# Performance work log

Hardware: AMD Instinct MI355X
Metric: run time of the kernel (lower is better)

## Reference

```python
import jax, jax.numpy as jnp
import numpy as np

VOCAB, DM, H, DH, FF, NL = 50265, 768, 12, 64, 3072, 12
WIN = 256  # one-sided window (attention_window=512)
B, S = 1, 4096


def layer_norm(x, s, b, eps=1e-5):
    mu = x.mean(-1, keepdims=True)
    var = x.var(-1, keepdims=True)
    return (x - mu) * jax.lax.rsqrt(var + eps) * s + b


def sliding_attn(x, key_mask, wq, wk, wv, bq, bk, bv):
    Bb, Ss, _ = x.shape
    nb = Ss // WIN
    q = ((x @ wq + bq) / np.float32(np.sqrt(DH))).reshape(Bb, nb, WIN, H, DH)
    k = (x @ wk + bk).reshape(Bb, Ss, H, DH)
    v = (x @ wv + bv).reshape(Bb, Ss, H, DH)
    pad = [(0, 0), (WIN, WIN), (0, 0), (0, 0)]
    kp = jnp.pad(k, pad).reshape(Bb, nb + 2, WIN, H, DH)
    vp = jnp.pad(v, pad).reshape(Bb, nb + 2, WIN, H, DH)
    mp = jnp.pad(key_mask, [(0, 0), (WIN, WIN)]).reshape(Bb, nb + 2, WIN)
    kwin = jnp.concatenate([kp[:, i:i + nb] for i in range(3)], axis=2)  # [B,nb,3W,H,DH]
    vwin = jnp.concatenate([vp[:, i:i + nb] for i in range(3)], axis=2)
    mwin = jnp.concatenate([mp[:, i:i + nb] for i in range(3)], axis=2)  # [B,nb,3W]
    scores = jnp.einsum('bnqhd,bnkhd->bhnqk', q, kwin)  # [B,H,nb,W,3W]
    rel = jnp.arange(3 * WIN)[None, :] - jnp.arange(WIN)[:, None]
    band = (rel >= 0) & (rel <= 2 * WIN)
    valid = band[None, None, None] & (mwin > 0)[:, None, :, None, :]
    probs = jax.nn.softmax(jnp.where(valid, scores, -1e9), axis=-1)
    out = jnp.einsum('bhnqk,bnkhd->bnqhd', probs, vwin)
    return out.reshape(Bb, Ss, H * DH)


def encode(tokens, mask, word_emb, pos_emb, emb_ln_s, emb_ln_b, qkv_w, qkv_b,
           attn_out_w, attn_out_b, attn_ln_s, attn_ln_b,
           ffn_w1, ffn_b1, ffn_w2, ffn_b2, ffn_ln_s, ffn_ln_b):
    Ss = tokens.shape[1]
    x = word_emb[tokens] + pos_emb[2:2 + Ss][None]  # roberta-style position offset
    x = layer_norm(x, emb_ln_s, emb_ln_b)
    for l in range(NL):
        a = sliding_attn(x, mask, qkv_w[l, 0], qkv_w[l, 1], qkv_w[l, 2],
                         qkv_b[l, 0], qkv_b[l, 1], qkv_b[l, 2])
        x = layer_norm(x + a @ attn_out_w[l] + attn_out_b[l], attn_ln_s[l], attn_ln_b[l])
        h = jax.nn.gelu(x @ ffn_w1[l] + ffn_b1[l], approximate=False)
        x = layer_norm(x + h @ ffn_w2[l] + ffn_b2[l], ffn_ln_s[l], ffn_ln_b[l])
    return x


def setup_inputs() -> dict:
    key = jax.random.key(0)
    ks = iter(jax.random.split(key, 40))
    tokens = jax.random.randint(next(ks), (B, 1, S), 0, VOCAB)
    mask = jnp.ones((B, 1, S), dtype=jnp.int64 if False else jnp.int32)
    essay_tokens = jnp.concatenate([tokens, mask.astype(tokens.dtype)], axis=1)
    g = lambda shape: (jax.random.normal(next(ks), shape, jnp.float32) * 0.02)
    return {
        'essay_tokens': essay_tokens,
        'word_emb': g((VOCAB, DM)), 'pos_emb': g((4098, DM)),
        'emb_ln_s': jnp.ones((DM,)), 'emb_ln_b': jnp.zeros((DM,)),
        'qkv_w': g((NL, 3, DM, DM)), 'qkv_b': g((NL, 3, DM)),
        'attn_out_w': g((NL, DM, DM)), 'attn_out_b': g((NL, DM)),
        'attn_ln_s': jnp.ones((NL, DM)), 'attn_ln_b': jnp.zeros((NL, DM)),
        'ffn_w1': g((NL, DM, FF)), 'ffn_b1': g((NL, FF)),
        'ffn_w2': g((NL, FF, DM)), 'ffn_b2': g((NL, DM)),
        'ffn_ln_s': jnp.ones((NL, DM)), 'ffn_ln_b': jnp.zeros((NL, DM)),
        'cls_w1': g((DM, 512)), 'cls_b1': jnp.zeros((512,)),
        'cls_w2': g((512, 512)), 'cls_b2': jnp.zeros((512,)),
        'cls_w3': g((512, 512)), 'cls_b3': jnp.zeros((512,)),
        'cls_w4': g((512, 2)), 'cls_b4': jnp.zeros((2,)),
    }


def reference(essay_tokens, word_emb, pos_emb, emb_ln_s, emb_ln_b, qkv_w, qkv_b,
              attn_out_w, attn_out_b, attn_ln_s, attn_ln_b,
              ffn_w1, ffn_b1, ffn_w2, ffn_b2, ffn_ln_s, ffn_ln_b,
              cls_w1, cls_b1, cls_w2, cls_b2, cls_w3, cls_b3, cls_w4, cls_b4):
    tokens = essay_tokens[:, 0, :].astype(jnp.int32)
    mask = essay_tokens[:, 1, :].astype(jnp.int32)
    enc = encode(tokens, mask, word_emb, pos_emb, emb_ln_s, emb_ln_b, qkv_w, qkv_b,
                 attn_out_w, attn_out_b, attn_ln_s, attn_ln_b,
                 ffn_w1, ffn_b1, ffn_w2, ffn_b2, ffn_ln_s, ffn_ln_b)
    # torch.no_grad() on the transformer
    enc = jax.lax.stop_gradient(enc)
    h = enc @ cls_w1 + cls_b1
    h = h @ cls_w2 + cls_b2
    h = h @ cls_w3 + cls_b3
    logits = h @ cls_w4 + cls_b4  # [B,S,2]
    out = logits[..., 0]          # chunk(..., 2, dim=-1)[0] then flatten(1)
    return out.reshape(out.shape[0], -1)
```

## Files before the change

### kernel.cpp

```cpp
#include <hip/hip_runtime.h>
#include <cmath>

#define S_LEN 4096
#define DMODEL 768
#define NHEAD 12
#define DHEAD 64
#define FFDIM 3072
#define NLAYER 12
#define WINR 256

typedef float f32x4 __attribute__((ext_vector_type(4)));
typedef short s8v __attribute__((ext_vector_type(8)));
typedef __bf16 b8v __attribute__((ext_vector_type(8)));

__device__ __forceinline__ short f2b(float f) {
  unsigned u = __builtin_bit_cast(unsigned, f);
  unsigned r = (u + 0x7fffu + ((u >> 16) & 1u)) >> 16;
  return (short)r;
}
__device__ __forceinline__ float b2f(short s) {
  unsigned u = ((unsigned)(unsigned short)s) << 16;
  return __builtin_bit_cast(float, u);
}
__device__ __forceinline__ f32x4 mfma16(s8v a, s8v b, f32x4 c) {
  return __builtin_amdgcn_mfma_f32_16x16x32_bf16(
      __builtin_bit_cast(b8v, a), __builtin_bit_cast(b8v, b), c, 0, 0, 0);
}
__device__ __forceinline__ void gl_lds16(const short* g, short* l) {
  __builtin_amdgcn_global_load_lds(
      (const __attribute__((address_space(1))) unsigned int*)g,
      (__attribute__((address_space(3))) unsigned int*)l, 16, 0, 0);
}

#define QSCALE 0.18033688011112042f
#define THR2 11.5415603f

__device__ __forceinline__ void wtr_tile(const float* __restrict__ src,
                                         short* __restrict__ dst, int K, int N,
                                         int k0, int n0, int t,
                                         short (*tile)[65]) {
  {
    int kr = t >> 2, nc = (t & 3) * 16;
    const float* p = src + (long)(k0 + kr) * N + n0 + nc;
#pragma unroll
    for (int q = 0; q < 4; ++q) {
      float4 f = *(const float4*)(p + q * 4);
      tile[kr][nc + q * 4 + 0] = f2b(f.x);
      tile[kr][nc + q * 4 + 1] = f2b(f.y);
      tile[kr][nc + q * 4 + 2] = f2b(f.z);
      tile[kr][nc + q * 4 + 3] = f2b(f.w);
    }
  }
  __syncthreads();
  {
    int nr = t >> 2, cc = (t & 3) * 16;
    short* q = dst + (long)(n0 + nr) * K + k0 + cc;
    s8v v0, v1;
#pragma unroll
    for (int j = 0; j < 8; ++j) v0[j] = tile[cc + j][nr];
#pragma unroll
    for (int j = 0; j < 8; ++j) v1[j] = tile[cc + 8 + j][nr];
    *(s8v*)q = v0;
    *(s8v*)(q + 8) = v1;
  }
}

__global__ __launch_bounds__(256) void wtr_kernel(const float* __restrict__ src,
                                                  short* __restrict__ dst,
                                                  int K, int N) {
  __shared__ short tile[64][65];
  wtr_tile(src, dst, K, N, blockIdx.y * 64, blockIdx.x * 64, threadIdx.x, tile);
}

__global__ __launch_bounds__(256) void wtr_layer_kernel(
    const float* __restrict__ qkv, const float* __restrict__ ao,
    const float* __restrict__ w1, const float* __restrict__ w2,
    short* __restrict__ lwq, short* __restrict__ lwa, short* __restrict__ lw1,
    short* __restrict__ lw2) {
  __shared__ short tile[64][65];
  const long DD = (long)DMODEL * DMODEL;
  int id = blockIdx.x;
  const float* src;
  short* dst;
  int K, N, nT, kT;
  if (id < 432) {
    int m = id / 144, r = id % 144;
    src = qkv + m * DD; dst = lwq + m * DD;
    K = DMODEL; N = DMODEL; nT = r % 12; kT = r / 12;
  } else if (id < 576) {
    int r = id - 432;
    src = ao; dst = lwa;
    K = DMODEL; N = DMODEL; nT = r % 12; kT = r / 12;
  } else if (id < 1152) {
    int r = id - 576;
    src = w1; dst = lw1;
    K = DMODEL; N = FFDIM; nT = r % 48; kT = r / 48;
  } else {
    int r = id - 1152;
    src = w2; dst = lw2;
    K = FFDIM; N = DMODEL; nT = r % 12; kT = r / 12;
  }
  wtr_tile(src, dst, K, N, kT * 64, nT * 64, threadIdx.x, tile);
}

__global__ __launch_bounds__(256) void vtr_kernel(const short* __restrict__ Vb,
                                                  short* __restrict__ VTg) {
  __shared__ short tile[64][65];
  const int s0 = blockIdx.x * 64, h = blockIdx.y;
  const int t = threadIdx.x;
  {
    int sr = t >> 2, dc = (t & 3) * 16;
    const short* p = Vb + (long)(s0 + sr) * DMODEL + h * 64 + dc;
    s8v a0 = *(const s8v*)p;
    s8v a1 = *(const s8v*)(p + 8);
#pragma unroll
    for (int j = 0; j < 8; ++j) tile[sr][dc + j] = a0[j];
#pragma unroll
    for (int j = 0; j < 8; ++j) tile[sr][dc + 8 + j] = a1[j];
  }
  __syncthreads();
  {
    int dr = t >> 2, sc = (t & 3) * 16;
    short* q = VTg + (long)(h * 64 + dr) * S_LEN + s0 + sc;
    s8v v0, v1;
#pragma unroll
    for (int j = 0; j < 8; ++j) v0[j] = tile[sc + j][dr];
#pragma unroll
    for (int j = 0; j < 8; ++j) v1[j] = tile[sc + 8 + j][dr];
    *(s8v*)q = v0;
    *(s8v*)(q + 8) = v1;
  }
}

template <int EPI, int OUT>
__global__ __launch_bounds__(256, 4) void bgemm_kernel(
    const short* __restrict__ A, const short* __restrict__ Bt,
    const float* __restrict__ bias, void* __restrict__ Cv,
    int N, int K, int Klen, long sB, long sBias, long sC) {
  __shared__ short As[2][128 * 32];
  __shared__ short Bs[2][128 * 32];
  const int t = threadIdx.x, lane = t & 63, w = t >> 6;
  const int lo = lane & 15, hi = lane >> 4;
  const int wm = (w >> 1) * 64, wn = (w & 1) * 64;

  const int gx = gridDim.x;
  const int bid = blockIdx.x + gx * (blockIdx.y + 32 * blockIdx.z);
  const int xcd = bid & 7;
  const int jj_ = bid >> 3;
  const int bx = jj_ % gx;
  const int t2 = jj_ / gx;
  const int by = xcd * 4 + (t2 & 3);
  const int bz = t2 >> 2;

  const long bm = (long)by * 128;
  const int bn = bx * 128;
  Bt += (long)bz * sB;
  const long Koff = (OUT == 2) ? (long)bz * Klen : 0;

  f32x4 acc[4][4];
#pragma unroll
  for (int i = 0; i < 4; ++i)
#pragma unroll
    for (int j = 0; j < 4; ++j) {
      f32x4 zz = {0.f, 0.f, 0.f, 0.f};
      acc[i][j] = zz;
    }

  const int srow = lane >> 2;
  const int schunk = (lane & 3) ^ ((lane >> 3) & 3);
  const short* ga = A + (bm + srow) * (long)K + Koff + schunk * 8;
  const short* gb = Bt + ((long)bn + srow) * K + Koff + schunk * 8;

#define STAGE(buf, koff)                                                   \
  {                                                                        \
    _Pragma("unroll") for (int i = 0; i < 2; ++i) {                        \
      const int r0 = i * 64 + w * 16;                                      \
      gl_lds16(ga + (long)r0 * K + (koff), As[buf] + r0 * 32);             \
      gl_lds16(gb + (long)r0 * K + (koff), Bs[buf] + r0 * 32);             \
    }                                                                      \
  }

  STAGE(0, 0);

  const int nt = Klen >> 5;
  const int rchunk = (hi ^ ((lo >> 1) & 3)) * 8;
  for (int kt = 0; kt < nt; ++kt) {
    const int cur = kt & 1;
    if (kt + 1 < nt) {
      STAGE(cur ^ 1, (kt + 1) * 32);
      asm volatile("s_waitcnt vmcnt(4)\n\ts_barrier" ::: "memory");
    } else {
      asm volatile("s_waitcnt vmcnt(0)\n\ts_barrier" ::: "memory");
    }
    s8v af[4], bf[4];
#pragma unroll
    for (int mi = 0; mi < 4; ++mi)
      af[mi] = *(const s8v*)(As[cur] + (wm + mi * 16 + lo) * 32 + rchunk);
#pragma unroll
    for (int ni = 0; ni < 4; ++ni)
      bf[ni] = *(const s8v*)(Bs[cur] + (wn + ni * 16 + lo) * 32 + rchunk);
#pragma unroll
    for (int mi = 0; mi < 4; ++mi)
#pragma unroll
      for (int ni = 0; ni < 4; ++ni)
        acc[mi][ni] = mfma16(af[mi], bf[ni], acc[mi][ni]);
    asm volatile("s_barrier" ::: "memory");
  }
#undef STAGE

  const float sc = (EPI == 2 && bz == 0) ? QSCALE : 1.0f;
  float* Cf = (float*)Cv + (long)bz * sC;
  short* Cs = (short*)Cv + (long)bz * sC;
  const float* bp = bias + (long)bz * sBias;
#pragma unroll
  for (int mi = 0; mi < 4; ++mi)
#pragma unroll
    for (int ni = 0; ni < 4; ++ni) {
      int col = bn + wn + ni * 16 + lo;
      float bb = (OUT == 2) ? 0.f : bp[col];
#pragma unroll
      for (int jj = 0; jj < 4; ++jj) {
        long row = bm + wm + mi * 16 + hi * 4 + jj;
        float v = acc[mi][ni][jj] + bb;
        if (EPI == 2) v *= sc;
        if (EPI == 1) v = 0.5f * v * (1.0f + erff(v * 0.7071067811865476f));
        if (OUT == 0)
          Cf[row * N + col] = v;
        else
          Cs[row * N + col] = f2b(v);
      }
    }
}

__global__ __launch_bounds__(256) void attn_kernel(
    const short* __restrict__ Qb, const short* __restrict__ Kb,
    const short* __restrict__ VTg, const int* __restrict__ maskp,
    short* __restrict__ Ob) {
  __shared__ short Ks[2][64 * 64];
  __shared__ short VT[2][64 * 64];
  __shared__ short Pl[4][16 * 64];
  __shared__ int mask_lds[576];

  const int t = threadIdx.x, lane = t & 63, w = t >> 6;
  const int lo = lane & 15, hi = lane >> 4;

  const int bid = blockIdx.x + 64 * blockIdx.y;
  const int xcd = bid & 7, jb = bid >> 3;
  const int qb = xcd * 8 + (jb & 7), h = jb >> 3;

  const int q0 = qb * 64;
  const int qw = q0 + w * 16;
  short* Plw = Pl[w];

  s8v aq[2];
#pragma unroll
  for (int kg = 0; kg < 2; ++kg)
    aq[kg] = *(const s8v*)(Qb + (long)(qw + lo) * DMODEL + h * 64 + kg * 32 +
                           hi * 8);

  f32x4 o[4];
#pragma unroll
  for (int i = 0; i < 4; ++i) {
    f32x4 zz = {0.f, 0.f, 0.f, 0.f};
    o[i] = zz;
  }
  float rm[4], rl[4];
#pragma unroll
  for (int r = 0; r < 4; ++r) { rm[r] = -1e30f; rl[r] = 0.f; }

  const int kstart = max(0, q0 - WINR);
  const int kend = min(S_LEN, q0 + 64 + WINR);
  const int nt = (kend - kstart) >> 6;

  for (int i = t; i < kend - kstart; i += 256) mask_lds[i] = maskp[kstart + i];
  __syncthreads();

  const int krow = lane >> 3;
  const int kxor = ((lane & 7) ^ krow) * 8;
  const long vrow = (long)(h * 64 + w * 16 + krow) * S_LEN;

#define STAGE_KV(buf, kt)                                                    \
  {                                                                          \
    _Pragma("unroll") for (int i = 0; i < 2; ++i) {                          \
      const int r0 = w * 16 + i * 8;                                         \
      gl_lds16(Kb + (long)((kt) + r0 + krow) * DMODEL + h * 64 + kxor,       \
               Ks[buf] + r0 * 64);                                           \
      gl_lds16(VTg + vrow + (long)i * 8 * S_LEN + (kt) + kxor,               \
               VT[buf] + r0 * 64);                                           \
    }                                                                        \
  }

  STAGE_KV(0, kstart);

  for (int ti = 0; ti < nt; ++ti) {
    const int kt = kstart + ti * 64;
    const int cur = ti & 1;
    if (ti + 1 < nt) {
      STAGE_KV(cur ^ 1, kt + 64);
      asm volatile("s_waitcnt vmcnt(4)\n\ts_barrier" ::: "memory");
    } else {
      asm volatile("s_waitcnt vmcnt(0)\n\ts_barrier" ::: "memory");
    }

    const bool active = (kt + 63 >= qw - WINR) && (kt <= qw + 15 + WINR);
    if (active) {
      f32x4 sacc[4];
#pragma unroll
      for (int i = 0; i < 4; ++i) {
        f32x4 zz = {0.f, 0.f, 0.f, 0.f};
        sacc[i] = zz;
      }
#pragma unroll
      for (int ni = 0; ni < 4; ++ni)
#pragma unroll
        for (int kg = 0; kg < 2; ++kg) {
          const int chunk = (kg * 4 + hi) ^ (lo & 7);
          s8v bk = *(const s8v*)(Ks[cur] + (ni * 16 + lo) * 64 + chunk * 8);
          sacc[ni] = mfma16(aq[kg], bk, sacc[ni]);
        }

      int mval[4];
#pragma unroll
      for (int ni = 0; ni < 4; ++ni)
        mval[ni] = mask_lds[kt - kstart + ni * 16 + lo];

      const bool fullband = (kt >= qw + 15 - WINR) && (kt + 63 <= qw + WINR);

      float m0[4];
      if (fullband) {
#pragma unroll
        for (int jj = 0; jj < 4; ++jj) {
          float mm = -1e30f;
#pragma unroll
          for (int ni = 0; ni < 4; ++ni) {
            float sv = (mval[ni] != 0) ? sacc[ni][jj] : -1e30f;
            sacc[ni][jj] = sv;
            mm = fmaxf(mm, sv);
          }
          mm = fmaxf(mm, __shfl_xor(mm, 1));
          mm = fmaxf(mm, __shfl_xor(mm, 2));
          mm = fmaxf(mm, __shfl_xor(mm, 4));
          mm = fmaxf(mm, __shfl_xor(mm, 8));
          m0[jj] = mm;
        }
      } else {
#pragma unroll
        for (int jj = 0; jj < 4; ++jj) {
          const int qg = qw + hi * 4 + jj;
          float mm = -1e30f;
#pragma unroll
          for (int ni = 0; ni < 4; ++ni) {
            int kg = kt + ni * 16 + lo;
            bool val = (kg >= qg - WINR) && (kg <= qg + WINR) && (mval[ni] != 0);
            float sv = val ? sacc[ni][jj] : -1e30f;
            sacc[ni][jj] = sv;
            mm = fmaxf(mm, sv);
          }
          mm = fmaxf(mm, __shfl_xor(mm, 1));
          mm = fmaxf(mm, __shfl_xor(mm, 2));
          mm = fmaxf(mm, __shfl_xor(mm, 4));
          mm = fmaxf(mm, __shfl_xor(mm, 8));
          m0[jj] = mm;
        }
      }

      bool skipf = true;
#pragma unroll
      for (int jj = 0; jj < 4; ++jj) skipf = skipf && (m0[jj] - rm[jj] <= THR2);

      if (__all(skipf)) {
#pragma unroll
        for (int jj = 0; jj < 4; ++jj) {
          float ts = 0.f;
#pragma unroll
          for (int ni = 0; ni < 4; ++ni) {
            float sv = sacc[ni][jj];
            float p = (sv > -1e29f) ? exp2f(sv - rm[jj]) : 0.f;
            sacc[ni][jj] = p;
            ts += p;
          }
          ts += __shfl_xor(ts, 1);
          ts += __shfl_xor(ts, 2);
          ts += __shfl_xor(ts, 4);
          ts += __shfl_xor(ts, 8);
          rl[jj] += ts;
        }
      } else {
#pragma unroll
        for (int jj = 0; jj < 4; ++jj) {
          float mnew = fmaxf(rm[jj], m0[jj]);
          float scl = exp2f(rm[jj] - mnew);
          rm[jj] = mnew;
          float ts = 0.f;
#pragma unroll
          for (int ni = 0; ni < 4; ++ni) {
            float sv = sacc[ni][jj];
            float p = (sv > -1e29f) ? exp2f(sv - mnew) : 0.f;
            sacc[ni][jj] = p;
            ts += p;
          }
          ts += __shfl_xor(ts, 1);
          ts += __shfl_xor(ts, 2);
          ts += __shfl_xor(ts, 4);
          ts += __shfl_xor(ts, 8);
          rl[jj] = rl[jj] * scl + ts;
#pragma unroll
          for (int di = 0; di < 4; ++di) o[di][jj] *= scl;
        }
      }

#pragma unroll
      for (int jj = 0; jj < 4; ++jj) {
        const int qr = hi * 4 + jj;
#pragma unroll
        for (int ni = 0; ni < 4; ++ni) {
          const int chunk = (ni * 2 + (lo >> 3)) ^ (qr & 7);
          Plw[qr * 64 + chunk * 8 + (lo & 7)] = f2b(sacc[ni][jj]);
        }
      }

      s8v ap[2];
#pragma unroll
      for (int kg = 0; kg < 2; ++kg) {
        const int chunk = (kg * 4 + hi) ^ (lo & 7);
        ap[kg] = *(const s8v*)(Plw + lo * 64 + chunk * 8);
      }
#pragma unroll
      for (int di = 0; di < 4; ++di)
#pragma unroll
        for (int kg = 0; kg < 2; ++kg) {
          const int chunk = (kg * 4 + hi) ^ (lo & 7);
          s8v bv = *(const s8v*)(VT[cur] + (di * 16 + lo) * 64 + chunk * 8);
          o[di] = mfma16(ap[kg], bv, o[di]);
        }
    }
    asm volatile("s_barrier" ::: "memory");
  }
#undef STAGE_KV

#pragma unroll
  for (int di = 0; di < 4; ++di)
#pragma unroll
    for (int jj = 0; jj < 4; ++jj) {
      long row = qw + hi * 4 + jj;
      Ob[row * DMODEL + h * 64 + di * 16 + lo] = f2b(o[di][jj] / rl[jj]);
    }
}

__global__ __launch_bounds__(256) void embed_ln_kernel(
    const int* __restrict__ tok, const float* __restrict__ wemb,
    const float* __restrict__ pemb, const float* __restrict__ gs,
    const float* __restrict__ gb, float* __restrict__ X,
    short* __restrict__ Xb) {
  __shared__ float sm1[4], sm2[4];
  const int row = blockIdx.x;
  const int tk = tok[row];
  float v[3];
  float s = 0.f, q = 0.f;
#pragma unroll
  for (int i = 0; i < 3; ++i) {
    int c = threadIdx.x + i * 256;
    float x = wemb[(long)tk * DMODEL + c] + pemb[(long)(row + 2) * DMODEL + c];
    v[i] = x;
    s += x;
    q += x * x;
  }
#pragma unroll
  for (int off = 32; off; off >>= 1) {
    s += __shfl_down(s, off);
    q += __shfl_down(q, off);
  }
  int w = threadIdx.x >> 6;
  if ((threadIdx.x & 63) == 0) { sm1[w] = s; sm2[w] = q; }
  __syncthreads();
  s = sm1[0] + sm1[1] + sm1[2] + sm1[3];
  q = sm2[0] + sm2[1] + sm2[2] + sm2[3];
  float mu = s * (1.f / DMODEL);
  float var = q * (1.f / DMODEL) - mu * mu;
  float inv = rsqrtf(var + 1e-5f);
#pragma unroll
  for (int i = 0; i < 3; ++i) {
    int c = threadIdx.x + i * 256;
    float y = (v[i] - mu) * inv * gs[c] + gb[c];
    X[(long)row * DMODEL + c] = y;
    Xb[(long)row * DMODEL + c] = f2b(y);
  }
}

__global__ __launch_bounds__(256) void resln2_kernel(
    float* __restrict__ X, const short* __restrict__ P0b,
    const short* __restrict__ P1b, const float* __restrict__ bias,
    const float* __restrict__ gs, const float* __restrict__ gb,
    short* __restrict__ Xb) {
  __shared__ float sm1[4], sm2[4];
  const int row = blockIdx.x;
  float v[3];
  float s = 0.f, q = 0.f;
#pragma unroll
  for (int i = 0; i < 3; ++i) {
    int c = threadIdx.x + i * 256;
    long ix = (long)row * DMODEL + c;
    float x = X[ix] + b2f(P0b[ix]) + b2f(P1b[ix]) + bias[c];
    v[i] = x;
    s += x;
    q += x * x;
  }
#pragma unroll
  for (int off = 32; off; off >>= 1) {
    s += __shfl_down(s, off);
    q += __shfl_down(q, off);
  }
  int w = threadIdx.x >> 6;
  if ((threadIdx.x & 63) == 0) { sm1[w] = s; sm2[w] = q; }
  __syncthreads();
  s = sm1[0] + sm1[1] + sm1[2] + sm1[3];
  q = sm2[0] + sm2[1] + sm2[2] + sm2[3];
  float mu = s * (1.f / DMODEL);
  float var = q * (1.f / DMODEL) - mu * mu;
  float inv = rsqrtf(var + 1e-5f);
#pragma unroll
  for (int i = 0; i < 3; ++i) {
    int c = threadIdx.x + i * 256;
    float y = (v[i] - mu) * inv * gs[c] + gb[c];
    X[(long)row * DMODEL + c] = y;
    Xb[(long)row * DMODEL + c] = f2b(y);
  }
}

__global__ __launch_bounds__(256) void cls_final_kernel(
    const short* __restrict__ Hh, const float* __restrict__ w4,
    const float* __restrict__ b4, float* __restrict__ out) {
  const int w = threadIdx.x >> 6, lane = threadIdx.x & 63;
  const int row = blockIdx.x * 4 + w;
  float s = 0.f;
#pragma unroll
  for (int j = 0; j < 8; ++j) {
    int k = lane + j * 64;
    s += b2f(Hh[(long)row * 512 + k]) * w4[k * 2];
  }
#pragma unroll
  for (int off = 32; off; off >>= 1) s += __shfl_down(s, off);
  if (lane == 0) out[row] = s + b4[0];
}

extern "C" void kernel_launch(void* const* d_in, const int* in_sizes, int n_in,
                              void* d_out, int out_size, void* d_ws,
                              size_t ws_size, hipStream_t stream) {
  const int* essay = (const int*)d_in[0];
  const float* wemb = (const float*)d_in[1];
  const float* pemb = (const float*)d_in[2];
  const float* eln_s = (const float*)d_in[3];
  const float* eln_b = (const float*)d_in[4];
  const float* qkv_w = (const float*)d_in[5];
  const float* qkv_b = (const float*)d_in[6];
  const float* aow = (const float*)d_in[7];
  const float* aob = (const float*)d_in[8];
  const float* aln_s = (const float*)d_in[9];
  const float* aln_b = (const float*)d_in[10];
  const float* w1 = (const float*)d_in[11];
  const float* b1 = (const float*)d_in[12];
  const float* w2 = (const float*)d_in[13];
  const float* b2 = (const float*)d_in[14];
  const float* fln_s = (const float*)d_in[15];
  const float* fln_b = (const float*)d_in[16];
  const float* c1w = (const float*)d_in[17];
  const float* c1b = (const float*)d_in[18];
  const float* c2w = (const float*)d_in[19];
  const float* c2b = (const float*)d_in[20];
  const float* c3w = (const float*)d_in[21];
  const float* c3b = (const float*)d_in[22];
  const float* c4w = (const float*)d_in[23];
  const float* c4b = (const float*)d_in[24];

  const long SD = (long)S_LEN * DMODEL;
  const long SF = (long)S_LEN * FFDIM;
  const long SH = (long)S_LEN * 512;
  const long DD = (long)DMODEL * DMODEL;
  const long DF = (long)DMODEL * FFDIM;

  float* X = (float*)d_ws;
  float* P0 = X + SD;
  float* P1 = P0 + SD;
  short* P0b = (short*)P0;
  short* P1b = P0b + SD;
  short* VTg = (short*)P1;
  short* lwq = (short*)(P1 + SD);
  short* lwa = lwq + 3 * DD;
  short* lw1 = lwa + DD;
  short* lw2 = lw1 + DF;
  short* c1T = lw2 + DF;
  short* c2T = c1T + (long)DMODEL * 512;
  short* c3T = c2T + 512L * 512;
  short* Xb = c3T + 512L * 512;
  short* QKVb = Xb + SD;
  short* T1b = QKVb + 3 * SD;
  short* T2b = T1b + SD;
  short* H1 = T2b + SF;
  short* H2 = H1 + SH;
  short* H3 = H2 + SH;
  const long needed = (char*)(H3 + SH) - (char*)d_ws;
  if (ws_size < (size_t)needed) return;

  const int* maskp = essay + S_LEN;

  embed_ln_kernel<<<S_LEN, 256, 0, stream>>>(essay, wemb, pemb, eln_s, eln_b, X,
                                             Xb);

  for (int l = 0; l < NLAYER; ++l) {
    wtr_layer_kernel<<<1728, 256, 0, stream>>>(
        qkv_w + l * 3 * DD, aow + l * DD, w1 + l * DF, w2 + l * DF, lwq, lwa,
        lw1, lw2);

    bgemm_kernel<2, 1><<<dim3(6, 32, 3), 256, 0, stream>>>(
        Xb, lwq, qkv_b + (long)l * 3 * DMODEL, QKVb, DMODEL, DMODEL, DMODEL, DD,
        DMODEL, SD);
    vtr_kernel<<<dim3(64, 12), 256, 0, stream>>>(QKVb + 2 * SD, VTg);
    attn_kernel<<<dim3(64, 12), 256, 0, stream>>>(QKVb, QKVb + SD, VTg, maskp,
                                                  T1b);
    bgemm_kernel<0, 2><<<dim3(6, 32, 2), 256, 0, stream>>>(
        T1b, lwa, aob, P0b, DMODEL, DMODEL, 384, 0, 0, SD);
    resln2_kernel<<<S_LEN, 256, 0, stream>>>(X, P0b, P1b,
                                             aob + (long)l * DMODEL,
                                             aln_s + (long)l * DMODEL,
                                             aln_b + (long)l * DMODEL, Xb);
    bgemm_kernel<1, 1><<<dim3(24, 32, 1), 256, 0, stream>>>(
        Xb, lw1, b1 + (long)l * FFDIM, T2b, FFDIM, DMODEL, DMODEL, 0, 0, 0);
    bgemm_kernel<0, 2><<<dim3(6, 32, 2), 256, 0, stream>>>(
        T2b, lw2, b2, P0b, DMODEL, FFDIM, 1536, 0, 0, SD);
    resln2_kernel<<<S_LEN, 256, 0, stream>>>(X, P0b, P1b,
                                             b2 + (long)l * DMODEL,
                                             fln_s + (long)l * DMODEL,
                                             fln_b + (long)l * DMODEL, Xb);
  }

  wtr_kernel<<<dim3(8, 12), 256, 0, stream>>>(c1w, c1T, DMODEL, 512);
  wtr_kernel<<<dim3(8, 8), 256, 0, stream>>>(c2w, c2T, 512, 512);
  wtr_kernel<<<dim3(8, 8), 256, 0, stream>>>(c3w, c3T, 512, 512);

  bgemm_kernel<0, 1><<<dim3(4, 32, 1), 256, 0, stream>>>(
      Xb, c1T, c1b, H1, 512, DMODEL, DMODEL, 0, 0, 0);
  bgemm_kernel<0, 1><<<dim3(4, 32, 1), 256, 0, stream>>>(H1, c2T, c2b, H2, 512,
                                                         512, 512, 0, 0, 0);
  bgemm_kernel<0, 1><<<dim3(4, 32, 1), 256, 0, stream>>>(H2, c3T, c3b, H3, 512,
                                                         512, 512, 0, 0, 0);
  cls_final_kernel<<<S_LEN / 4, 256, 0, stream>>>(H3, c4w, c4b, (float*)d_out);
}
```

Baseline: 2.103 ms.

## Fuse V transpose into QKV GEMM epilogue and drop fp32 residual stream

The QKV GEMM now writes the V slice already transposed, staging it through a swizzled shared-memory tile, so the separate V-transpose kernel is no longer launched each layer. The fp32 residual copy X is also removed: layer norms read and write only the bf16 activations. This saves a launch and a round trip through global memory for V, plus fp32 residual reads and writes in every layer norm. The cost is that the residual stream is carried in bf16 across all layers, which can add numerical error.

Result: faster. 1.914 ms (-9.0%).

```diff
diff --git a/kernel.cpp b/kernel.cpp
--- a/kernel.cpp
+++ b/kernel.cpp
@@ -10,6 +10,7 @@
 #define WINR 256
 
 typedef float f32x4 __attribute__((ext_vector_type(4)));
+typedef short s4v __attribute__((ext_vector_type(4)));
 typedef short s8v __attribute__((ext_vector_type(8)));
 typedef __bf16 b8v __attribute__((ext_vector_type(8)));
 
@@ -103,42 +104,12 @@
   wtr_tile(src, dst, K, N, kT * 64, nT * 64, threadIdx.x, tile);
 }
 
-__global__ __launch_bounds__(256) void vtr_kernel(const short* __restrict__ Vb,
-                                                  short* __restrict__ VTg) {
-  __shared__ short tile[64][65];
-  const int s0 = blockIdx.x * 64, h = blockIdx.y;
-  const int t = threadIdx.x;
-  {
-    int sr = t >> 2, dc = (t & 3) * 16;
-    const short* p = Vb + (long)(s0 + sr) * DMODEL + h * 64 + dc;
-    s8v a0 = *(const s8v*)p;
-    s8v a1 = *(const s8v*)(p + 8);
-#pragma unroll
-    for (int j = 0; j < 8; ++j) tile[sr][dc + j] = a0[j];
-#pragma unroll
-    for (int j = 0; j < 8; ++j) tile[sr][dc + 8 + j] = a1[j];
-  }
-  __syncthreads();
-  {
-    int dr = t >> 2, sc = (t & 3) * 16;
-    short* q = VTg + (long)(h * 64 + dr) * S_LEN + s0 + sc;
-    s8v v0, v1;
-#pragma unroll
-    for (int j = 0; j < 8; ++j) v0[j] = tile[sc + j][dr];
-#pragma unroll
-    for (int j = 0; j < 8; ++j) v1[j] = tile[sc + 8 + j][dr];
-    *(s8v*)q = v0;
-    *(s8v*)(q + 8) = v1;
-  }
-}
-
 template <int EPI, int OUT>
 __global__ __launch_bounds__(256, 4) void bgemm_kernel(
     const short* __restrict__ A, const short* __restrict__ Bt,
     const float* __restrict__ bias, void* __restrict__ Cv,
     int N, int K, int Klen, long sB, long sBias, long sC) {
-  __shared__ short As[2][128 * 32];
-  __shared__ short Bs[2][128 * 32];
+  __shared__ short smem[16384];
   const int t = threadIdx.x, lane = t & 63, w = t >> 6;
   const int lo = lane & 15, hi = lane >> 4;
   const int wm = (w >> 1) * 64, wn = (w & 1) * 64;
@@ -171,13 +142,14 @@
   const short* ga = A + (bm + srow) * (long)K + Koff + schunk * 8;
   const short* gb = Bt + ((long)bn + srow) * K + Koff + schunk * 8;
 
-#define STAGE(buf, koff)                                                   \
-  {                                                                        \
-    _Pragma("unroll") for (int i = 0; i < 2; ++i) {                        \
-      const int r0 = i * 64 + w * 16;                                      \
-      gl_lds16(ga + (long)r0 * K + (koff), As[buf] + r0 * 32);             \
-      gl_lds16(gb + (long)r0 * K + (koff), Bs[buf] + r0 * 32);             \
-    }                                                                      \
+#define STAGE(buf, koff)                                                     \
+  {                                                                          \
+    _Pragma("unroll") for (int i = 0; i < 2; ++i) {                          \
+      const int r0 = i * 64 + w * 16;                                        \
+      gl_lds16(ga + (long)r0 * K + (koff), smem + (buf)*4096 + r0 * 32);     \
+      gl_lds16(gb + (long)r0 * K + (koff),                                   \
+               smem + 8192 + (buf)*4096 + r0 * 32);                          \
+    }                                                                        \
   }
 
   STAGE(0, 0);
@@ -195,10 +167,12 @@
     s8v af[4], bf[4];
 #pragma unroll
     for (int mi = 0; mi < 4; ++mi)
-      af[mi] = *(const s8v*)(As[cur] + (wm + mi * 16 + lo) * 32 + rchunk);
+      af[mi] = *(const s8v*)(smem + cur * 4096 + (wm + mi * 16 + lo) * 32 +
+                             rchunk);
 #pragma unroll
     for (int ni = 0; ni < 4; ++ni)
-      bf[ni] = *(const s8v*)(Bs[cur] + (wn + ni * 16 + lo) * 32 + rchunk);
+      bf[ni] = *(const s8v*)(smem + 8192 + cur * 4096 +
+                             (wn + ni * 16 + lo) * 32 + rchunk);
 #pragma unroll
     for (int mi = 0; mi < 4; ++mi)
 #pragma unroll
@@ -212,6 +186,34 @@
   float* Cf = (float*)Cv + (long)bz * sC;
   short* Cs = (short*)Cv + (long)bz * sC;
   const float* bp = bias + (long)bz * sBias;
+
+  if (OUT == 3 && bz == 2) {
+    short* T = smem;
+#pragma unroll
+    for (int mi = 0; mi < 4; ++mi)
+#pragma unroll
+      for (int ni = 0; ni < 4; ++ni) {
+        const int cl = wn + ni * 16 + lo;
+        const float bb = bp[bn + cl];
+        const int rb = wm + mi * 16 + hi * 4;
+        const int rs = rb ^ ((cl & 15) << 3);
+        s4v v;
+#pragma unroll
+        for (int jj = 0; jj < 4; ++jj) v[jj] = f2b(acc[mi][ni][jj] + bb);
+        *(s4v*)&T[cl * 128 + rs] = v;
+      }
+    __syncthreads();
+#pragma unroll
+    for (int it = 0; it < 8; ++it) {
+      const int id = t + it * 256;
+      const int col = id >> 4;
+      const int r8 = (id & 15) * 8;
+      s8v vv = *(const s8v*)&T[col * 128 + (r8 ^ ((col & 15) << 3))];
+      *(s8v*)(Cs + (long)(bn + col) * S_LEN + bm + r8) = vv;
+    }
+    return;
+  }
+
 #pragma unroll
   for (int mi = 0; mi < 4; ++mi)
 #pragma unroll
@@ -450,8 +452,7 @@
 __global__ __launch_bounds__(256) void embed_ln_kernel(
     const int* __restrict__ tok, const float* __restrict__ wemb,
     const float* __restrict__ pemb, const float* __restrict__ gs,
-    const float* __restrict__ gb, float* __restrict__ X,
-    short* __restrict__ Xb) {
+    const float* __restrict__ gb, short* __restrict__ Xb) {
   __shared__ float sm1[4], sm2[4];
   const int row = blockIdx.x;
   const int tk = tok[row];
@@ -482,16 +483,14 @@
   for (int i = 0; i < 3; ++i) {
     int c = threadIdx.x + i * 256;
     float y = (v[i] - mu) * inv * gs[c] + gb[c];
-    X[(long)row * DMODEL + c] = y;
     Xb[(long)row * DMODEL + c] = f2b(y);
   }
 }
 
 __global__ __launch_bounds__(256) void resln2_kernel(
-    float* __restrict__ X, const short* __restrict__ P0b,
+    short* __restrict__ Xb, const short* __restrict__ P0b,
     const short* __restrict__ P1b, const float* __restrict__ bias,
-    const float* __restrict__ gs, const float* __restrict__ gb,
-    short* __restrict__ Xb) {
+    const float* __restrict__ gs, const float* __restrict__ gb) {
   __shared__ float sm1[4], sm2[4];
   const int row = blockIdx.x;
   float v[3];
@@ -500,7 +499,7 @@
   for (int i = 0; i < 3; ++i) {
     int c = threadIdx.x + i * 256;
     long ix = (long)row * DMODEL + c;
-    float x = X[ix] + b2f(P0b[ix]) + b2f(P1b[ix]) + bias[c];
+    float x = b2f(Xb[ix]) + b2f(P0b[ix]) + b2f(P1b[ix]) + bias[c];
     v[i] = x;
     s += x;
     q += x * x;
@@ -522,7 +521,6 @@
   for (int i = 0; i < 3; ++i) {
     int c = threadIdx.x + i * 256;
     float y = (v[i] - mu) * inv * gs[c] + gb[c];
-    X[(long)row * DMODEL + c] = y;
     Xb[(long)row * DMODEL + c] = f2b(y);
   }
 }
@@ -578,13 +576,9 @@
   const long DD = (long)DMODEL * DMODEL;
   const long DF = (long)DMODEL * FFDIM;
 
-  float* X = (float*)d_ws;
-  float* P0 = X + SD;
-  float* P1 = P0 + SD;
-  short* P0b = (short*)P0;
+  short* P0b = (short*)d_ws;
   short* P1b = P0b + SD;
-  short* VTg = (short*)P1;
-  short* lwq = (short*)(P1 + SD);
+  short* lwq = P1b + SD;
   short* lwa = lwq + 3 * DD;
   short* lw1 = lwa + DD;
   short* lw2 = lw1 + DF;
@@ -603,7 +597,7 @@
 
   const int* maskp = essay + S_LEN;
 
-  embed_ln_kernel<<<S_LEN, 256, 0, stream>>>(essay, wemb, pemb, eln_s, eln_b, X,
+  embed_ln_kernel<<<S_LEN, 256, 0, stream>>>(essay, wemb, pemb, eln_s, eln_b,
                                              Xb);
 
   for (int l = 0; l < NLAYER; ++l) {
@@ -611,26 +605,25 @@
         qkv_w + l * 3 * DD, aow + l * DD, w1 + l * DF, w2 + l * DF, lwq, lwa,
         lw1, lw2);
 
-    bgemm_kernel<2, 1><<<dim3(6, 32, 3), 256, 0, stream>>>(
+    bgemm_kernel<2, 3><<<dim3(6, 32, 3), 256, 0, stream>>>(
         Xb, lwq, qkv_b + (long)l * 3 * DMODEL, QKVb, DMODEL, DMODEL, DMODEL, DD,
         DMODEL, SD);
-    vtr_kernel<<<dim3(64, 12), 256, 0, stream>>>(QKVb + 2 * SD, VTg);
-    attn_kernel<<<dim3(64, 12), 256, 0, stream>>>(QKVb, QKVb + SD, VTg, maskp,
-                                                  T1b);
+    attn_kernel<<<dim3(64, 12), 256, 0, stream>>>(QKVb, QKVb + SD,
+                                                  QKVb + 2 * SD, maskp, T1b);
     bgemm_kernel<0, 2><<<dim3(6, 32, 2), 256, 0, stream>>>(
         T1b, lwa, aob, P0b, DMODEL, DMODEL, 384, 0, 0, SD);
-    resln2_kernel<<<S_LEN, 256, 0, stream>>>(X, P0b, P1b,
+    resln2_kernel<<<S_LEN, 256, 0, stream>>>(Xb, P0b, P1b,
                                              aob + (long)l * DMODEL,
                                              aln_s + (long)l * DMODEL,
-                                             aln_b + (long)l * DMODEL, Xb);
+                                             aln_b + (long)l * DMODEL);
     bgemm_kernel<1, 1><<<dim3(24, 32, 1), 256, 0, stream>>>(
         Xb, lw1, b1 + (long)l * FFDIM, T2b, FFDIM, DMODEL, DMODEL, 0, 0, 0);
     bgemm_kernel<0, 2><<<dim3(6, 32, 2), 256, 0, stream>>>(
         T2b, lw2, b2, P0b, DMODEL, FFDIM, 1536, 0, 0, SD);
-    resln2_kernel<<<S_LEN, 256, 0, stream>>>(X, P0b, P1b,
+    resln2_kernel<<<S_LEN, 256, 0, stream>>>(Xb, P0b, P1b,
                                              b2 + (long)l * DMODEL,
                                              fln_s + (long)l * DMODEL,
-                                             fln_b + (long)l * DMODEL, Xb);
+                                             fln_b + (long)l * DMODEL);
   }
 
   wtr_kernel<<<dim3(8, 12), 256, 0, stream>>>(c1w, c1T, DMODEL, 512);
```
